# Kernel tuning notes

Measured on AMD Instinct MI355X. Metric: run time of the kernel, lower is better.

The kernel has to match this reference:

```python
import jax, jax.numpy as jnp
import numpy as np

N_USERS, N_ITEMS, D = 16384, 8192, 64
IMG_D, TXT_D = 4096, 384
TOPK = 10
LAMBDA = 0.9         # args.lambda_coeff
NNZ = 786432
N_TOTAL = N_USERS + N_ITEMS


def l2norm(x, eps=1e-12):
    # F.normalize(p=2, dim=1)
    return x / jnp.maximum(jnp.linalg.norm(x, axis=-1, keepdims=True), eps)


def build_knn_graph(feats):
    """build_sim + build_knn_normalized_graph (sparse, sym norm).
    Returns row-sparse KNN graph as (values [N,k], indices [N,k])."""
    z = l2norm(feats)
    sim = z @ z.T                          # [N, N] cosine similarity
    vals, inds = jax.lax.top_k(sim, TOPK)  # [N, k]
    rowsum = vals.sum(axis=1)              # degree
    d_inv_sqrt = jnp.where(rowsum > 0, rowsum, 1.0) ** -0.5
    vals = vals * d_inv_sqrt[:, None] * d_inv_sqrt[inds]  # D^-1/2 A D^-1/2
    return vals, inds


def knn_mm(vals, inds, x):
    # sparse.mm with row-sparse [N,k] graph: out[i] = sum_k vals[i,k]*x[inds[i,k]]
    return jnp.einsum('nk,nkd->nd', vals, x[inds])


def setup_inputs() -> dict:
    key = jax.random.key(0)
    ks = jax.random.split(key, 16)
    xav = lambda k, shp: jax.random.normal(k, shp, jnp.float32) * (2.0 / (shp[0] + shp[-1])) ** 0.5
    return dict(
        adj_rows=jax.random.randint(ks[0], (NNZ,), 0, N_TOTAL, jnp.int32),
        adj_cols=jax.random.randint(ks[1], (NNZ,), 0, N_TOTAL, jnp.int32),
        adj_vals=jax.random.uniform(ks[2], (NNZ,), jnp.float32) / 32.0,
        image_feats=jax.random.normal(ks[3], (N_ITEMS, IMG_D), jnp.float32),
        text_feats=jax.random.normal(ks[4], (N_ITEMS, TXT_D), jnp.float32),
        user_emb=xav(ks[5], (N_USERS, D)),
        item_emb=xav(ks[6], (N_ITEMS, D)),
        img_w=xav(ks[7], (IMG_D, D)), img_b=jnp.zeros((D,), jnp.float32),
        txt_w=xav(ks[8], (TXT_D, D)), txt_b=jnp.zeros((D,), jnp.float32),
        q_w1=xav(ks[9], (D, D)), q_b1=jnp.zeros((D,), jnp.float32),
        q_w2=xav(ks[10], (D, 1)),
        gc_w=xav(ks[11], (2, D, D)), gc_b=jnp.zeros((2, D), jnp.float32),
        bi_w=xav(ks[12], (2, D, D)), bi_b=jnp.zeros((2, D), jnp.float32),
    )


def reference(adj_rows, adj_cols, adj_vals, image_feats, text_feats,
              user_emb, item_emb, img_w, img_b, txt_w, txt_b,
              q_w1, q_b1, q_w2, gc_w, gc_b, bi_w, bi_b):
    # original (init-time) modal graphs from raw features
    io_v, io_i = build_knn_graph(image_feats)
    to_v, to_i = build_knn_graph(text_feats)
    # projected modal features + dynamic graphs (build_item_graph=True)
    img_f = image_feats @ img_w + img_b
    txt_f = text_feats @ txt_w + txt_b
    in_v, in_i = build_knn_graph(img_f)
    tn_v, tn_i = build_knn_graph(txt_f)
    # one propagation layer over (1-l)*new_adj + l*orig_adj (separable for layers=1)
    e = item_emb
    img_e = (1 - LAMBDA) * knn_mm(in_v, in_i, e) + LAMBDA * knn_mm(io_v, io_i, e)
    txt_e = (1 - LAMBDA) * knn_mm(tn_v, tn_i, e) + LAMBDA * knn_mm(to_v, to_i, e)
    # attention-weighted fusion
    query = lambda x: jnp.tanh(x @ q_w1 + q_b1) @ q_w2   # [N_ITEMS, 1]
    att = jnp.concatenate([query(img_e), query(txt_e)], axis=-1)
    w = jax.nn.softmax(att, axis=-1)
    h = w[:, :1] * img_e + w[:, 1:] * txt_e
    # NGCF user-item propagation (dropout p=0 -> identity)
    ego = jnp.concatenate([user_emb, item_emb], axis=0)   # [N_TOTAL, D]
    all_e = [ego]
    for i in range(2):
        side = jax.ops.segment_sum(adj_vals[:, None] * ego[adj_cols], adj_rows,
                                   num_segments=N_TOTAL)
        s = jax.nn.leaky_relu(side @ gc_w[i] + gc_b[i])
        b = jax.nn.leaky_relu((ego * side) @ bi_w[i] + bi_b[i])
        ego = s + b
        all_e.append(l2norm(ego))
    all_e = jnp.mean(jnp.stack(all_e, axis=1), axis=1)
    u_g, i_g = all_e[:N_USERS], all_e[N_USERS:]
    i_g = i_g + l2norm(h)
    return u_g, i_g, img_e, txt_e, h
```

## Files before the change

### kernel.cpp

```cpp
#include <hip/hip_runtime.h>
#include <hip/hip_bf16.h>
#include <math.h>

#define N_USERS 16384
#define N_ITEMS 8192
#define N_TOTAL 24576
#define EMB_D 64
#define IMG_DIM 4096
#define TXT_DIM 384
#define K_TOP 10
#define N_CAND 16
#define NNZ_E 786432

typedef _Float16 f16x8 __attribute__((ext_vector_type(8)));
typedef float f32x4 __attribute__((ext_vector_type(4)));

#define AS1 __attribute__((address_space(1)))
#define AS3 __attribute__((address_space(3)))

__device__ __forceinline__ float leaky01(float x){ return x >= 0.f ? x : 0.01f * x; }

__device__ __forceinline__ void gld16(const void* g, void* l) {
  __builtin_amdgcn_global_load_lds((const AS1 unsigned int*)g, (AS3 unsigned int*)l, 16, 0, 0);
}

__device__ __forceinline__ bool beats(float v, int i, float u, int j) {
  return v > u || (v == u && i < j);
}

__device__ __forceinline__ float h2f(unsigned short u) {
  _Float16 h = __builtin_bit_cast(_Float16, u);
  return (float)h;
}

__global__ __launch_bounds__(256) void norm_cast_fused_k(const float* __restrict__ x,
                                                         float* __restrict__ invn,
                                                         unsigned short* __restrict__ zh, int K) {
  __shared__ __align__(16) float xr[4096];
  __shared__ float red[256];
  int r = blockIdx.x;
  const float* xp = x + (size_t)r * K;
  float ss = 0.f;
  for (int j = threadIdx.x; j < K; j += 256) { float v = xp[j]; xr[j] = v; ss += v * v; }
  red[threadIdx.x] = ss; __syncthreads();
  for (int s = 128; s > 0; s >>= 1) {
    if (threadIdx.x < s) red[threadIdx.x] += red[threadIdx.x + s];
    __syncthreads();
  }
  float inv = 1.f / fmaxf(sqrtf(red[0]), 1e-12f);
  if (threadIdx.x == 0) invn[r] = inv;
  for (int j = threadIdx.x; j < K; j += 256) {
    _Float16 h = (_Float16)(xr[j] * inv);
    zh[(size_t)r * K + j] = __builtin_bit_cast(unsigned short, h);
  }
}

__global__ __launch_bounds__(256) void sim_mfma_k(const unsigned short* __restrict__ Zh,
                                                  unsigned short* __restrict__ C, int K, int r0) {
  __shared__ unsigned short smA[128 * 32];
  __shared__ unsigned short smB[128 * 32];
  const int tid = threadIdx.x;
  const int lane = tid & 63;
  const int wid = tid >> 6;
  const int wr = wid >> 1, wc = wid & 1;

  const int nx = gridDim.x;
  const int nwg = nx * gridDim.y;
  const int wg = blockIdx.y * nx + blockIdx.x;
  const int cpx = nwg >> 3;
  const int swz = (wg & 7) * cpx + (wg >> 3);
  const int tileX = swz % nx, tileY = swz / nx;

  const int bRow = r0 + tileY * 128;
  const int bCol = tileX * 128;

  f32x4 acc[4][4];
  const f32x4 fzero = {0.f, 0.f, 0.f, 0.f};
  #pragma unroll
  for (int m = 0; m < 4; m++)
    #pragma unroll
    for (int n = 0; n < 4; n++) acc[m][n] = fzero;

  const int u0 = (wid * 2 + 0) * 64 + lane;
  const int u1 = (wid * 2 + 1) * 64 + lane;
  const int ar0 = u0 >> 2, ac0 = (u0 & 3) * 8;
  const int ar1 = u1 >> 2, ac1 = (u1 & 3) * 8;
  const size_t rowA0 = (size_t)(bRow + ar0) * K;
  const size_t rowA1 = (size_t)(bRow + ar1) * K;
  const size_t rowB0 = (size_t)(bCol + ar0) * K;
  const size_t rowB1 = (size_t)(bCol + ar1) * K;
  unsigned short* ldsA0 = smA + (wid * 2 + 0) * 512;
  unsigned short* ldsA1 = smA + (wid * 2 + 1) * 512;
  unsigned short* ldsB0 = smB + (wid * 2 + 0) * 512;
  unsigned short* ldsB1 = smB + (wid * 2 + 1) * 512;

  const int kc = lane >> 4;
  const int fr = lane & 15;

  for (int k0 = 0; k0 < K; k0 += 32) {
    __syncthreads();
    gld16(Zh + rowA0 + k0 + ac0, ldsA0);
    gld16(Zh + rowA1 + k0 + ac1, ldsA1);
    gld16(Zh + rowB0 + k0 + ac0, ldsB0);
    gld16(Zh + rowB1 + k0 + ac1, ldsB1);
    __syncthreads();

    f16x8 a[4], b[4];
    #pragma unroll
    for (int m = 0; m < 4; m++)
      a[m] = *(const f16x8*)&smA[(wr * 64 + m * 16 + fr) * 32 + kc * 8];
    #pragma unroll
    for (int n = 0; n < 4; n++)
      b[n] = *(const f16x8*)&smB[(wc * 64 + n * 16 + fr) * 32 + kc * 8];
    #pragma unroll
    for (int m = 0; m < 4; m++)
      #pragma unroll
      for (int n = 0; n < 4; n++)
        acc[m][n] = __builtin_amdgcn_mfma_f32_16x16x32_f16(a[m], b[n], acc[m][n], 0, 0, 0);
  }

  const int crow = tileY * 128 + wr * 64 + (lane >> 4) * 4;
  const int ccol = bCol + wc * 64 + (lane & 15);
  #pragma unroll
  for (int m = 0; m < 4; m++)
    #pragma unroll
    for (int n = 0; n < 4; n++)
      #pragma unroll
      for (int r = 0; r < 4; r++) {
        _Float16 hv = (_Float16)acc[m][n][r];
        C[(size_t)(crow + m * 16 + r) * N_ITEMS + ccol + n * 16] =
            __builtin_bit_cast(unsigned short, hv);
      }
}

__device__ __forceinline__ void ins4(float val, int idx, float tv[4], int ti[4]) {
  if (beats(val, idx, tv[3], ti[3])) {
    tv[3] = val; ti[3] = idx;
    if (beats(tv[3], ti[3], tv[2], ti[2])) { float a=tv[2];int b=ti[2]; tv[2]=tv[3];ti[2]=ti[3]; tv[3]=a;ti[3]=b; }
    if (beats(tv[2], ti[2], tv[1], ti[1])) { float a=tv[1];int b=ti[1]; tv[1]=tv[2];ti[1]=ti[2]; tv[2]=a;ti[2]=b; }
    if (beats(tv[1], ti[1], tv[0], ti[0])) { float a=tv[0];int b=ti[0]; tv[0]=tv[1];ti[0]=ti[1]; tv[1]=a;ti[1]=b; }
  }
}

__global__ __launch_bounds__(256) void topk16h_k(const unsigned short* __restrict__ sim,
                                                 int r0, int* __restrict__ cand) {
  int row = blockIdx.x * 4 + (threadIdx.x >> 6);
  int lane = threadIdx.x & 63;
  const uint4* s8 = reinterpret_cast<const uint4*>(sim + (size_t)row * N_ITEMS);

  float tv[4]; int ti[4];
  #pragma unroll
  for (int k = 0; k < 4; k++) { tv[k] = -INFINITY; ti[k] = 0x7fffffff; }
  unsigned long long ext0 = 0ull, ext1 = 0ull;

  for (int i = 0; i < 16; i++) {
    uint4 v = s8[i * 64 + lane];
    int base = (i * 64 + lane) * 8;
    ins4(h2f(v.x & 0xffff), base + 0, tv, ti);
    ins4(h2f(v.x >> 16),    base + 1, tv, ti);
    ins4(h2f(v.y & 0xffff), base + 2, tv, ti);
    ins4(h2f(v.y >> 16),    base + 3, tv, ti);
    ins4(h2f(v.z & 0xffff), base + 4, tv, ti);
    ins4(h2f(v.z >> 16),    base + 5, tv, ti);
    ins4(h2f(v.w & 0xffff), base + 6, tv, ti);
    ins4(h2f(v.w >> 16),    base + 7, tv, ti);
  }
  int nvalid = 4;
  for (int t = 0; t < N_CAND; t++) {
    float bv = tv[0]; int bi = ti[0];
    for (int o = 32; o; o >>= 1) {
      float ov = __shfl_xor(bv, o, 64);
      int   oi = __shfl_xor(bi, o, 64);
      if (beats(ov, oi, bv, bi)) { bv = ov; bi = oi; }
    }
    if (tv[0] == bv && ti[0] == bi) {
      int slot = ((bi >> 9) << 3) | (bi & 7);
      if (slot < 64) ext0 |= 1ull << slot; else ext1 |= 1ull << (slot - 64);
      tv[0]=tv[1];ti[0]=ti[1]; tv[1]=tv[2];ti[1]=ti[2]; tv[2]=tv[3];ti[2]=ti[3];
      tv[3]=-INFINITY; ti[3]=0x7fffffff;
      nvalid--;
      if (nvalid == 0) {
        for (int i = 0; i < 16; i++) {
          uint4 v = s8[i * 64 + lane];
          int base = (i * 64 + lane) * 8;
          float vv[8] = {h2f(v.x & 0xffff), h2f(v.x >> 16), h2f(v.y & 0xffff), h2f(v.y >> 16),
                         h2f(v.z & 0xffff), h2f(v.z >> 16), h2f(v.w & 0xffff), h2f(v.w >> 16)};
          #pragma unroll
          for (int q = 0; q < 8; q++) {
            int slot2 = i * 8 + q;
            bool used = (slot2 < 64) ? ((ext0 >> slot2) & 1ull) : ((ext1 >> (slot2 - 64)) & 1ull);
            if (!used) ins4(vv[q], base + q, tv, ti);
          }
        }
        nvalid = 4;
      }
    }
    if (lane == 0) cand[(size_t)(r0 + row) * N_CAND + t] = bi;
  }
}

__global__ __launch_bounds__(256) void refine_k(const float* __restrict__ X, int K,
                                                const float* __restrict__ invn,
                                                const int* __restrict__ cand,
                                                float* __restrict__ vals, int* __restrict__ inds,
                                                float* __restrict__ dis) {
  __shared__ __align__(16) float xr[4096];
  __shared__ float dots[N_CAND];
  int row = blockIdx.x;
  int tid = threadIdx.x, lane = tid & 63, wid = tid >> 6;
  for (int j = tid; j < K; j += 256) xr[j] = X[(size_t)row * K + j];
  __syncthreads();
  for (int c = wid; c < N_CAND; c += 4) {
    int ci = cand[(size_t)row * N_CAND + c];
    const float* xc = X + (size_t)ci * K;
    float p = 0.f;
    if (K == 4096) {
      const float4* xc4 = reinterpret_cast<const float4*>(xc);
      const float4* xr4 = reinterpret_cast<const float4*>(xr);
      for (int it = 0; it < 16; it++) {
        float4 a = xr4[it * 64 + lane];
        float4 g = xc4[it * 64 + lane];
        p += a.x * g.x + a.y * g.y + a.z * g.z + a.w * g.w;
      }
    } else {
      for (int j = lane; j < K; j += 64) p += xr[j] * xc[j];
    }
    for (int o = 32; o; o >>= 1) p += __shfl_xor(p, o, 64);
    if (lane == 0) dots[c] = p;
  }
  __syncthreads();
  if (tid == 0) {
    float v[N_CAND]; int id[N_CAND];
    float ir = invn[row];
    for (int c = 0; c < N_CAND; c++) {
      id[c] = cand[(size_t)row * N_CAND + c];
      v[c] = dots[c] * ir * invn[id[c]];
    }
    for (int a = 1; a < N_CAND; a++) {
      float av = v[a]; int ai = id[a];
      int b = a - 1;
      while (b >= 0 && beats(av, ai, v[b], id[b])) { v[b+1]=v[b]; id[b+1]=id[b]; b--; }
      v[b+1] = av; id[b+1] = ai;
    }
    float sum = 0.f;
    for (int t = 0; t < K_TOP; t++) {
      vals[(size_t)row * K_TOP + t] = v[t];
      inds[(size_t)row * K_TOP + t] = id[t];
      sum += v[t];
    }
    float rs = sum > 0.f ? sum : 1.0f;
    dis[row] = 1.0f / sqrtf(rs);
  }
}

__global__ __launch_bounds__(256) void scale_vals_k(float* __restrict__ vals,
                                                    const int* __restrict__ inds,
                                                    const float* __restrict__ dis, int tot) {
  int idx = blockIdx.x * 256 + threadIdx.x;
  if (idx < tot) {
    int i = idx / K_TOP;
    vals[idx] *= dis[i] * dis[inds[idx]];
  }
}

__global__ __launch_bounds__(256) void linear_splitk_k(const float* __restrict__ X,
                                                       const float* __restrict__ W,
                                                       const float* __restrict__ b,
                                                       float* __restrict__ outp, int K, int KS) {
  __shared__ float As[64][17];
  __shared__ float Ws[16][64];
  int br = blockIdx.x, ks = blockIdx.y;
  int tid = threadIdx.x, tr = tid >> 4, tc = tid & 15;
  int k0 = ks * KS, k1 = k0 + KS;
  int lrow = tid >> 2, lk = (tid & 3) * 4;
  int wrow = tid >> 4, wcol = (tid & 15) * 4;
  float acc[4][4] = {};
  for (int kb = k0; kb < k1; kb += 16) {
    __syncthreads();
    float4 xv = *(const float4*)&X[(size_t)(br * 64 + lrow) * K + kb + lk];
    As[lrow][lk + 0] = xv.x; As[lrow][lk + 1] = xv.y;
    As[lrow][lk + 2] = xv.z; As[lrow][lk + 3] = xv.w;
    *(float4*)&Ws[wrow][wcol] = *(const float4*)&W[(size_t)(kb + wrow) * 64 + wcol];
    __syncthreads();
    #pragma unroll
    for (int k = 0; k < 16; k++) {
      float a[4], w[4];
      #pragma unroll
      for (int i = 0; i < 4; i++) a[i] = As[tr * 4 + i][k];
      #pragma unroll
      for (int j = 0; j < 4; j++) w[j] = Ws[k][tc * 4 + j];
      #pragma unroll
      for (int i = 0; i < 4; i++)
        #pragma unroll
        for (int j = 0; j < 4; j++) acc[i][j] += a[i] * w[j];
    }
  }
  #pragma unroll
  for (int i = 0; i < 4; i++)
    #pragma unroll
    for (int j = 0; j < 4; j++) {
      float v = acc[i][j];
      if (ks == 0) v += b[tc * 4 + j];
      atomicAdd(&outp[(size_t)(br * 64 + tr * 4 + i) * 64 + tc * 4 + j], v);
    }
}

__global__ __launch_bounds__(256) void fuse_knn_k(const float* __restrict__ av, const int* __restrict__ ai,
                                                  const float* __restrict__ bv, const int* __restrict__ bi_,
                                                  const float* __restrict__ e, float* __restrict__ outp,
                                                  float lam) {
  int i = blockIdx.x * 4 + (threadIdx.x >> 6), d = threadIdx.x & 63;
  float sa = 0.f, sb = 0.f;
  #pragma unroll
  for (int k = 0; k < K_TOP; k++) {
    sa += av[(size_t)i * K_TOP + k] * e[(size_t)ai[(size_t)i * K_TOP + k] * 64 + d];
    sb += bv[(size_t)i * K_TOP + k] * e[(size_t)bi_[(size_t)i * K_TOP + k] * 64 + d];
  }
  outp[(size_t)i * 64 + d] = (1.f - lam) * sa + lam * sb;
}

__global__ __launch_bounds__(64) void attn_k(const float* __restrict__ img_e, const float* __restrict__ txt_e,
                                             const float* __restrict__ qw1, const float* __restrict__ qb1,
                                             const float* __restrict__ qw2, float* __restrict__ h) {
  __shared__ float W1[64][64];
  __shared__ float sI[64], sT[64];
  int t = threadIdx.x; int i = blockIdx.x;
  for (int k = 0; k < 64; k++) W1[k][t] = qw1[k * 64 + t];
  sI[t] = img_e[(size_t)i * 64 + t];
  sT[t] = txt_e[(size_t)i * 64 + t];
  __syncthreads();
  float yi = qb1[t], yt = qb1[t];
  #pragma unroll 16
  for (int k = 0; k < 64; k++) { yi += sI[k] * W1[k][t]; yt += sT[k] * W1[k][t]; }
  float w2 = qw2[t];
  float pi = tanhf(yi) * w2, pt = tanhf(yt) * w2;
  for (int o = 32; o > 0; o >>= 1) { pi += __shfl_xor(pi, o, 64); pt += __shfl_xor(pt, o, 64); }
  float m = fmaxf(pi, pt);
  float ei = expf(pi - m), et = expf(pt - m);
  float den = ei + et;
  float w0 = ei / den, w1v = et / den;
  h[(size_t)i * 64 + t] = w0 * sI[t] + w1v * sT[t];
}

__global__ __launch_bounds__(256) void scatter_k(const int* __restrict__ rows, const int* __restrict__ cols,
                                                 const float* __restrict__ vals, const float* __restrict__ ego,
                                                 float* __restrict__ side) {
  int e = blockIdx.x * 4 + (threadIdx.x >> 6);
  int d = threadIdx.x & 63;
  float v = vals[e];
  int c = cols[e], r = rows[e];
  atomicAdd(&side[(size_t)r * 64 + d], v * ego[(size_t)c * 64 + d]);
}

__global__ __launch_bounds__(256) void gcn_k(const float* __restrict__ side, const float* __restrict__ ego,
                                             const float* __restrict__ gw, const float* __restrict__ gb,
                                             const float* __restrict__ bw, const float* __restrict__ bb,
                                             float* __restrict__ outp) {
  __shared__ float W1[64][64], W2[64][64];
  __shared__ float S[4][64], E[4][64];
  int t = threadIdx.x & 63, rb = threadIdx.x >> 6;
  int r = blockIdx.x * 4 + rb;
  for (int idx = threadIdx.x; idx < 4096; idx += 256) {
    W1[idx >> 6][idx & 63] = gw[idx];
    W2[idx >> 6][idx & 63] = bw[idx];
  }
  S[rb][t] = side[(size_t)r * 64 + t];
  E[rb][t] = ego[(size_t)r * 64 + t];
  __syncthreads();
  float s = gb[t], b = bb[t];
  #pragma unroll 16
  for (int k = 0; k < 64; k++) {
    float sv = S[rb][k];
    s += sv * W1[k][t];
    b += E[rb][k] * sv * W2[k][t];
  }
  outp[(size_t)r * 64 + t] = leaky01(s) + leaky01(b);
}

__global__ __launch_bounds__(256) void l2acc_k(const float* __restrict__ ego, float* __restrict__ acc) {
  int r = blockIdx.x * 4 + (threadIdx.x >> 6), d = threadIdx.x & 63;
  float v = ego[(size_t)r * 64 + d];
  float ss = v * v;
  for (int o = 32; o > 0; o >>= 1) ss += __shfl_xor(ss, o, 64);
  float inv = 1.f / fmaxf(sqrtf(ss), 1e-12f);
  acc[(size_t)r * 64 + d] += v * inv;
}

__global__ __launch_bounds__(256) void init_ego_k(const float* __restrict__ ue, const float* __restrict__ ie,
                                                  float* __restrict__ ego, float* __restrict__ acc) {
  int r = blockIdx.x * 4 + (threadIdx.x >> 6), d = threadIdx.x & 63;
  float v = (r < N_USERS) ? ue[(size_t)r * 64 + d] : ie[(size_t)(r - N_USERS) * 64 + d];
  ego[(size_t)r * 64 + d] = v;
  acc[(size_t)r * 64 + d] = v;
}

__global__ __launch_bounds__(256) void final_k(const float* __restrict__ acc, const float* __restrict__ h,
                                               float* __restrict__ u_g, float* __restrict__ i_g) {
  int r = blockIdx.x * 4 + (threadIdx.x >> 6), d = threadIdx.x & 63;
  float m = acc[(size_t)r * 64 + d] * (1.0f / 3.0f);
  if (r < N_USERS) {
    u_g[(size_t)r * 64 + d] = m;
  } else {
    int i = r - N_USERS;
    float hv = h[(size_t)i * 64 + d];
    float ss = hv * hv;
    for (int o = 32; o > 0; o >>= 1) ss += __shfl_xor(ss, o, 64);
    float inv = 1.f / fmaxf(sqrtf(ss), 1e-12f);
    i_g[(size_t)i * 64 + d] = m + hv * inv;
  }
}

static void build_graph(hipStream_t stream, const float* feats, int K, float* invn,
                        unsigned short* zh, unsigned short* sim, int stripe, int* cand,
                        float* vals, int* inds, float* dis) {
  norm_cast_fused_k<<<N_ITEMS, 256, 0, stream>>>(feats, invn, zh, K);
  for (int r0 = 0; r0 < N_ITEMS; r0 += stripe) {
    int rows = (N_ITEMS - r0) < stripe ? (N_ITEMS - r0) : stripe;
    dim3 g(N_ITEMS / 128, rows / 128);
    sim_mfma_k<<<g, 256, 0, stream>>>(zh, sim, K, r0);
    topk16h_k<<<rows / 4, 256, 0, stream>>>(sim, r0, cand);
  }
  refine_k<<<N_ITEMS, 256, 0, stream>>>(feats, K, invn, cand, vals, inds, dis);
  int tot = N_ITEMS * K_TOP;
  scale_vals_k<<<(tot + 255) / 256, 256, 0, stream>>>(vals, inds, dis, tot);
}

extern "C" void kernel_launch(void* const* d_in, const int* in_sizes, int n_in,
                              void* d_out, int out_size, void* d_ws, size_t ws_size,
                              hipStream_t stream) {
  const int*   adj_rows   = (const int*)d_in[0];
  const int*   adj_cols   = (const int*)d_in[1];
  const float* adj_vals   = (const float*)d_in[2];
  const float* image_feats= (const float*)d_in[3];
  const float* text_feats = (const float*)d_in[4];
  const float* user_emb   = (const float*)d_in[5];
  const float* item_emb   = (const float*)d_in[6];
  const float* img_w      = (const float*)d_in[7];
  const float* img_b      = (const float*)d_in[8];
  const float* txt_w      = (const float*)d_in[9];
  const float* txt_b      = (const float*)d_in[10];
  const float* q_w1       = (const float*)d_in[11];
  const float* q_b1       = (const float*)d_in[12];
  const float* q_w2       = (const float*)d_in[13];
  const float* gc_w       = (const float*)d_in[14];
  const float* gc_b       = (const float*)d_in[15];
  const float* bi_w       = (const float*)d_in[16];
  const float* bi_b       = (const float*)d_in[17];

  float* out  = (float*)d_out;
  float* u_g  = out;
  float* i_g  = u_g + (size_t)N_USERS * 64;
  float* imgE = i_g + (size_t)N_ITEMS * 64;
  float* txtE = imgE + (size_t)N_ITEMS * 64;
  float* hOut = txtE + (size_t)N_ITEMS * 64;

  float* W = (float*)d_ws;
  size_t off = 0;
  auto alloc = [&](size_t n) { float* q = W + off; off += n; return q; };
  float* inv_io = alloc(N_ITEMS);
  float* inv_to = alloc(N_ITEMS);
  float* inv_in = alloc(N_ITEMS);
  float* inv_tn = alloc(N_ITEMS);
  float* img_f  = alloc((size_t)N_ITEMS * 64);
  float* txt_f  = alloc((size_t)N_ITEMS * 64);
  float* vals0 = alloc(N_ITEMS * K_TOP); int* inds0 = (int*)alloc(N_ITEMS * K_TOP);
  float* vals1 = alloc(N_ITEMS * K_TOP); int* inds1 = (int*)alloc(N_ITEMS * K_TOP);
  float* vals2 = alloc(N_ITEMS * K_TOP); int* inds2 = (int*)alloc(N_ITEMS * K_TOP);
  float* vals3 = alloc(N_ITEMS * K_TOP); int* inds3 = (int*)alloc(N_ITEMS * K_TOP);
  float* dis0 = alloc(N_ITEMS);
  float* dis1 = alloc(N_ITEMS);
  float* dis2 = alloc(N_ITEMS);
  float* dis3 = alloc(N_ITEMS);
  int*   cand = (int*)alloc((size_t)N_ITEMS * N_CAND);
  float* ego_a = alloc((size_t)N_TOTAL * 64);
  float* ego_b = alloc((size_t)N_TOTAL * 64);
  float* side  = alloc((size_t)N_TOTAL * 64);
  float* acc   = alloc((size_t)N_TOTAL * 64);
  unsigned short* zh = (unsigned short*)alloc(((size_t)N_ITEMS * IMG_DIM) / 2);
  unsigned short* sim = (unsigned short*)(W + off);

  size_t used_bytes = off * 4;
  size_t avail_b = (ws_size > used_bytes) ? (ws_size - used_bytes) : 0;
  long stripe_l = (long)((avail_b / ((size_t)N_ITEMS * 2)) / 128) * 128;
  if (stripe_l > N_ITEMS) stripe_l = N_ITEMS;
  if (stripe_l < 128) stripe_l = 128;
  int stripe = (int)stripe_l;

  build_graph(stream, image_feats, IMG_DIM, inv_io, zh, sim, stripe, cand, vals0, inds0, dis0);
  build_graph(stream, text_feats,  TXT_DIM, inv_to, zh, sim, stripe, cand, vals1, inds1, dis1);

  hipMemsetAsync(img_f, 0, (size_t)N_ITEMS * 64 * sizeof(float), stream);
  hipMemsetAsync(txt_f, 0, (size_t)N_ITEMS * 64 * sizeof(float), stream);
  linear_splitk_k<<<dim3(N_ITEMS / 64, 4), 256, 0, stream>>>(image_feats, img_w, img_b, img_f, IMG_DIM, IMG_DIM / 4);
  linear_splitk_k<<<dim3(N_ITEMS / 64, 4), 256, 0, stream>>>(text_feats,  txt_w, txt_b, txt_f, TXT_DIM, TXT_DIM / 4);

  build_graph(stream, img_f, 64, inv_in, zh, sim, stripe, cand, vals2, inds2, dis2);
  build_graph(stream, txt_f, 64, inv_tn, zh, sim, stripe, cand, vals3, inds3, dis3);

  const float lam = 0.9f;
  fuse_knn_k<<<N_ITEMS / 4, 256, 0, stream>>>(vals2, inds2, vals0, inds0, item_emb, imgE, lam);
  fuse_knn_k<<<N_ITEMS / 4, 256, 0, stream>>>(vals3, inds3, vals1, inds1, item_emb, txtE, lam);

  attn_k<<<N_ITEMS, 64, 0, stream>>>(imgE, txtE, q_w1, q_b1, q_w2, hOut);

  init_ego_k<<<N_TOTAL / 4, 256, 0, stream>>>(user_emb, item_emb, ego_a, acc);

  hipMemsetAsync(side, 0, (size_t)N_TOTAL * 64 * sizeof(float), stream);
  scatter_k<<<NNZ_E / 4, 256, 0, stream>>>(adj_rows, adj_cols, adj_vals, ego_a, side);
  gcn_k<<<N_TOTAL / 4, 256, 0, stream>>>(side, ego_a, gc_w, gc_b, bi_w, bi_b, ego_b);
  l2acc_k<<<N_TOTAL / 4, 256, 0, stream>>>(ego_b, acc);

  hipMemsetAsync(side, 0, (size_t)N_TOTAL * 64 * sizeof(float), stream);
  scatter_k<<<NNZ_E / 4, 256, 0, stream>>>(adj_rows, adj_cols, adj_vals, ego_b, side);
  gcn_k<<<N_TOTAL / 4, 256, 0, stream>>>(side, ego_b, gc_w + 4096, gc_b + 64, bi_w + 4096, bi_b + 64, ego_a);
  l2acc_k<<<N_TOTAL / 4, 256, 0, stream>>>(ego_a, acc);

  final_k<<<N_TOTAL / 4, 256, 0, stream>>>(acc, hOut, u_g, i_g);
}
```

Measured before the change: 2.665 ms.

## Build CSR for adjacency to replace atomic scatter; stage sim epilogue through LDS

Builds a CSR ordering of the edge list (histogram, single-block scan, atomic placement) once per call and replaces the two atomic scatter passes with a per-row gather that writes side directly, removing the memsets and atomic contention. The similarity GEMM epilogue now stages fp16 results in padded shared memory and writes 16-byte coalesced rows instead of scattered 2-byte stores. The grid tile swizzle is also removed. The CSR build adds extra kernels including a serial-ish one-block scan, and placement order is nondeterministic, so the floating-point summation order varies from run to run.

New measurement: 2.847 ms. +6.9%, slower.

```diff
diff --git a/kernel.cpp b/kernel.cpp
--- a/kernel.cpp
+++ b/kernel.cpp
@@ -55,24 +55,18 @@
   }
 }
 
+#define EPI_LD 136
 __global__ __launch_bounds__(256) void sim_mfma_k(const unsigned short* __restrict__ Zh,
                                                   unsigned short* __restrict__ C, int K, int r0) {
-  __shared__ unsigned short smA[128 * 32];
-  __shared__ unsigned short smB[128 * 32];
+  __shared__ __align__(16) unsigned short smem[128 * EPI_LD];
+  unsigned short* smA = smem;
+  unsigned short* smB = smem + 128 * 32;
   const int tid = threadIdx.x;
   const int lane = tid & 63;
   const int wid = tid >> 6;
   const int wr = wid >> 1, wc = wid & 1;
-
-  const int nx = gridDim.x;
-  const int nwg = nx * gridDim.y;
-  const int wg = blockIdx.y * nx + blockIdx.x;
-  const int cpx = nwg >> 3;
-  const int swz = (wg & 7) * cpx + (wg >> 3);
-  const int tileX = swz % nx, tileY = swz / nx;
-
-  const int bRow = r0 + tileY * 128;
-  const int bCol = tileX * 128;
+  const int bRow = r0 + blockIdx.y * 128;
+  const int bCol = blockIdx.x * 128;
 
   f32x4 acc[4][4];
   const f32x4 fzero = {0.f, 0.f, 0.f, 0.f};
@@ -119,8 +113,9 @@
         acc[m][n] = __builtin_amdgcn_mfma_f32_16x16x32_f16(a[m], b[n], acc[m][n], 0, 0, 0);
   }
 
-  const int crow = tileY * 128 + wr * 64 + (lane >> 4) * 4;
-  const int ccol = bCol + wc * 64 + (lane & 15);
+  __syncthreads();
+  const int lr = wr * 64 + (lane >> 4) * 4;
+  const int lc = wc * 64 + (lane & 15);
   #pragma unroll
   for (int m = 0; m < 4; m++)
     #pragma unroll
@@ -128,9 +123,17 @@
       #pragma unroll
       for (int r = 0; r < 4; r++) {
         _Float16 hv = (_Float16)acc[m][n][r];
-        C[(size_t)(crow + m * 16 + r) * N_ITEMS + ccol + n * 16] =
-            __builtin_bit_cast(unsigned short, hv);
+        smem[(lr + m * 16 + r) * EPI_LD + lc + n * 16] = __builtin_bit_cast(unsigned short, hv);
       }
+  __syncthreads();
+  const int outRow0 = blockIdx.y * 128;
+  #pragma unroll
+  for (int i = 0; i < 8; i++) {
+    int idx = i * 2048 + tid * 8;
+    int rr = idx >> 7, cc = idx & 127;
+    *(uint4*)&C[(size_t)(outRow0 + rr) * N_ITEMS + bCol + cc] =
+        *(const uint4*)&smem[rr * EPI_LD + cc];
+  }
 }
 
 __device__ __forceinline__ void ins4(float val, int idx, float tv[4], int ti[4]) {
@@ -342,14 +345,61 @@
   h[(size_t)i * 64 + t] = w0 * sI[t] + w1v * sT[t];
 }
 
-__global__ __launch_bounds__(256) void scatter_k(const int* __restrict__ rows, const int* __restrict__ cols,
-                                                 const float* __restrict__ vals, const float* __restrict__ ego,
-                                                 float* __restrict__ side) {
-  int e = blockIdx.x * 4 + (threadIdx.x >> 6);
+__global__ __launch_bounds__(256) void hist_k(const int* __restrict__ rows, int* __restrict__ cnt) {
+  int e = blockIdx.x * 256 + threadIdx.x;
+  if (e < NNZ_E) atomicAdd(&cnt[rows[e]], 1);
+}
+
+__global__ __launch_bounds__(256) void scan_k(const int* __restrict__ cnt,
+                                              int* __restrict__ starts,
+                                              int* __restrict__ cursor) {
+  __shared__ int part[256];
+  int t = threadIdx.x;
+  int base = t * (N_TOTAL / 256);
+  int s = 0;
+  for (int j = 0; j < N_TOTAL / 256; j++) s += cnt[base + j];
+  part[t] = s;
+  __syncthreads();
+  for (int off = 1; off < 256; off <<= 1) {
+    int v = part[t];
+    int u = (t >= off) ? part[t - off] : 0;
+    __syncthreads();
+    part[t] = v + u;
+    __syncthreads();
+  }
+  int run = (t > 0) ? part[t - 1] : 0;
+  for (int j = 0; j < N_TOTAL / 256; j++) {
+    starts[base + j] = run;
+    cursor[base + j] = run;
+    run += cnt[base + j];
+  }
+  if (t == 255) starts[N_TOTAL] = run;
+}
+
+__global__ __launch_bounds__(256) void place_k(const int* __restrict__ rows,
+                                               int* __restrict__ cursor, int* __restrict__ perm) {
+  int e = blockIdx.x * 256 + threadIdx.x;
+  if (e < NNZ_E) {
+    int p = atomicAdd(&cursor[rows[e]], 1);
+    perm[p] = e;
+  }
+}
+
+__global__ __launch_bounds__(256) void gather_gcn_k(const int* __restrict__ starts,
+                                                    const int* __restrict__ perm,
+                                                    const int* __restrict__ cols,
+                                                    const float* __restrict__ vals,
+                                                    const float* __restrict__ ego,
+                                                    float* __restrict__ side) {
+  int row = blockIdx.x * 4 + (threadIdx.x >> 6);
   int d = threadIdx.x & 63;
-  float v = vals[e];
-  int c = cols[e], r = rows[e];
-  atomicAdd(&side[(size_t)r * 64 + d], v * ego[(size_t)c * 64 + d]);
+  int s = starts[row], e = starts[row + 1];
+  float acc = 0.f;
+  for (int i = s; i < e; i++) {
+    int eid = perm[i];
+    acc += vals[eid] * ego[(size_t)cols[eid] * 64 + d];
+  }
+  side[(size_t)row * 64 + d] = acc;
 }
 
 __global__ __launch_bounds__(256) void gcn_k(const float* __restrict__ side, const float* __restrict__ ego,
@@ -476,6 +526,10 @@
   float* ego_b = alloc((size_t)N_TOTAL * 64);
   float* side  = alloc((size_t)N_TOTAL * 64);
   float* acc   = alloc((size_t)N_TOTAL * 64);
+  int* csr_cnt    = (int*)alloc(N_TOTAL);
+  int* csr_starts = (int*)alloc(N_TOTAL + 1);
+  int* csr_cursor = (int*)alloc(N_TOTAL);
+  int* csr_perm   = (int*)alloc(NNZ_E);
   unsigned short* zh = (unsigned short*)alloc(((size_t)N_ITEMS * IMG_DIM) / 2);
   unsigned short* sim = (unsigned short*)(W + off);
 
@@ -486,6 +540,11 @@
   if (stripe_l < 128) stripe_l = 128;
   int stripe = (int)stripe_l;
 
+  hipMemsetAsync(csr_cnt, 0, N_TOTAL * sizeof(int), stream);
+  hist_k<<<(NNZ_E + 255) / 256, 256, 0, stream>>>(adj_rows, csr_cnt);
+  scan_k<<<1, 256, 0, stream>>>(csr_cnt, csr_starts, csr_cursor);
+  place_k<<<(NNZ_E + 255) / 256, 256, 0, stream>>>(adj_rows, csr_cursor, csr_perm);
+
   build_graph(stream, image_feats, IMG_DIM, inv_io, zh, sim, stripe, cand, vals0, inds0, dis0);
   build_graph(stream, text_feats,  TXT_DIM, inv_to, zh, sim, stripe, cand, vals1, inds1, dis1);
 
@@ -505,13 +564,11 @@
 
   init_ego_k<<<N_TOTAL / 4, 256, 0, stream>>>(user_emb, item_emb, ego_a, acc);
 
-  hipMemsetAsync(side, 0, (size_t)N_TOTAL * 64 * sizeof(float), stream);
-  scatter_k<<<NNZ_E / 4, 256, 0, stream>>>(adj_rows, adj_cols, adj_vals, ego_a, side);
+  gather_gcn_k<<<N_TOTAL / 4, 256, 0, stream>>>(csr_starts, csr_perm, adj_cols, adj_vals, ego_a, side);
   gcn_k<<<N_TOTAL / 4, 256, 0, stream>>>(side, ego_a, gc_w, gc_b, bi_w, bi_b, ego_b);
   l2acc_k<<<N_TOTAL / 4, 256, 0, stream>>>(ego_b, acc);
 
-  hipMemsetAsync(side, 0, (size_t)N_TOTAL * 64 * sizeof(float), stream);
-  scatter_k<<<NNZ_E / 4, 256, 0, stream>>>(adj_rows, adj_cols, adj_vals, ego_b, side);
+  gather_gcn_k<<<N_TOTAL / 4, 256, 0, stream>>>(csr_starts, csr_perm, adj_cols, adj_vals, ego_b, side);
   gcn_k<<<N_TOTAL / 4, 256, 0, stream>>>(side, ego_b, gc_w + 4096, gc_b + 64, bi_w + 4096, bi_b + 64, ego_a);
   l2acc_k<<<N_TOTAL / 4, 256, 0, stream>>>(ego_a, acc);
 
```
